# Kernel optimization log

Hardware: AMD Instinct MI355X
Metric: run time of the kernel (lower is better)

Reference implementation:

```python
import jax, jax.numpy as jnp
import numpy as np

D_MODEL = 1024
N_HEAD = 16
HEAD_D = D_MODEL // N_HEAD
D_FF = 4096
LN_EPS = 1e-5
ATTN_EPS = 1e-6


def _layer_norm(x, g, b, eps=LN_EPS):
    mu = jnp.mean(x, axis=-1, keepdims=True)
    var = jnp.var(x, axis=-1, keepdims=True)
    return (x - mu) * jax.lax.rsqrt(var + eps) * g + b


def setup_inputs() -> dict:
    key = jax.random.key(0)
    ks = jax.random.split(key, 16)
    s = 0.02
    return {
        "src": jax.random.normal(ks[0], (4, 4096, D_MODEL), dtype=jnp.float32),
        "qkv_w": jax.random.normal(ks[1], (D_MODEL, 3 * D_MODEL), dtype=jnp.float32) * s,
        "qkv_b": jax.random.normal(ks[2], (3 * D_MODEL,), dtype=jnp.float32) * s,
        "out_w": jax.random.normal(ks[3], (D_MODEL, D_MODEL), dtype=jnp.float32) * s,
        "out_b": jax.random.normal(ks[4], (D_MODEL,), dtype=jnp.float32) * s,
        "w1": jax.random.normal(ks[5], (D_MODEL, D_FF), dtype=jnp.float32) * s,
        "b1": jax.random.normal(ks[6], (D_FF,), dtype=jnp.float32) * s,
        "w2": jax.random.normal(ks[7], (D_FF, D_MODEL), dtype=jnp.float32) * s,
        "b2": jax.random.normal(ks[8], (D_MODEL,), dtype=jnp.float32) * s,
        "g1": jnp.ones((D_MODEL,), dtype=jnp.float32),
        "be1": jnp.zeros((D_MODEL,), dtype=jnp.float32),
        "g2": jnp.ones((D_MODEL,), dtype=jnp.float32),
        "be2": jnp.zeros((D_MODEL,), dtype=jnp.float32),
    }


def _linear_attention(x, qkv_w, qkv_b, out_w, out_b):
    B, N, C = x.shape
    qkv = (x @ qkv_w + qkv_b).reshape(B, N, 3, N_HEAD, HEAD_D)
    qkv = jnp.transpose(qkv, (2, 0, 3, 1, 4))  # [3,B,H,N,D]
    q, k, v = qkv[0], qkv[1], qkv[2]
    # phi = elu(x) + 1 (positive feature map)
    qf = jax.nn.elu(q) + 1.0
    kf = jax.nn.elu(k) + 1.0
    # kv aggregation: [B,H,D,D]
    kv = jnp.einsum('bhnd,bhne->bhde', kf.astype(jnp.float32), v.astype(jnp.float32)).astype(v.dtype)
    y_num = jnp.einsum('bhnd,bhde->bhne', qf, kv)  # [B,H,N,D]
    z = jnp.sum(kf.astype(jnp.float32), axis=2)  # [B,H,D]
    y_den = jnp.einsum('bhnd,bhd->bhn', qf, z.astype(qf.dtype))
    y_den = jnp.maximum(y_den, ATTN_EPS)[..., None]
    y = (y_num / y_den).transpose(0, 2, 1, 3).reshape(B, N, C)
    return y @ out_w + out_b


def reference(src, qkv_w, qkv_b, out_w, out_b, w1, b1, w2, b2, g1, be1, g2, be2):
    # pre-norm (norm_first=True), dropout disabled (eval)
    attn_out = _linear_attention(_layer_norm(src, g1, be1), qkv_w, qkv_b, out_w, out_b)
    x = src + attn_out
    h = jax.nn.gelu(_layer_norm(x, g2, be2) @ w1 + b1, approximate=False)
    return x + h @ w2 + b2
```

## Files before the change

kernel.cpp:

```cpp
#include <hip/hip_runtime.h>
#include <hip/hip_bf16.h>
#include <math.h>

typedef __attribute__((ext_vector_type(8))) short short8;
typedef __attribute__((ext_vector_type(4))) float floatx4;

__device__ __forceinline__ float bf2f(unsigned int u) {
    union { unsigned int i; float f; } c; c.i = u << 16; return c.f;
}
__device__ __forceinline__ unsigned short f2bf(float f) {
    unsigned int x = __builtin_bit_cast(unsigned int, f);
    unsigned int r = (x + 0x7fffu + ((x >> 16) & 1u)) >> 16;
    return (unsigned short)r;
}
__device__ __forceinline__ float elu1(float x) { return x > 0.f ? x + 1.f : __expf(x); }
__device__ __forceinline__ float gelu_fast(float x) {
    float u = x * (1.f + 0.044715f * x * x);
    return x / (1.f + __expf(-1.5957691216f * u));
}

__device__ __forceinline__ void async_cp16(const void* g, void* l) {
    __builtin_amdgcn_global_load_lds(
        (const __attribute__((address_space(1))) unsigned int*)g,
        (__attribute__((address_space(3))) unsigned int*)l, 16, 0, 0);
}

__global__ void prep_kernel(const float* __restrict__ qkv_w, const float* __restrict__ out_w,
                            const float* __restrict__ w1, const float* __restrict__ w2,
                            unsigned short* __restrict__ qkvwT, unsigned short* __restrict__ outwT,
                            unsigned short* __restrict__ w1T, unsigned short* __restrict__ w2T,
                            float* __restrict__ kvz,
                            const float* __restrict__ src, const float* __restrict__ g1,
                            const float* __restrict__ be1, unsigned short* __restrict__ ln1out) {
    const int bid = blockIdx.x;
    const int tx = threadIdx.x, ty = threadIdx.y;
    const int lid = ty * 32 + tx;
    if (bid >= 12548) {
        const int row = bid - 12548;
        const int t = lid;
        const float4 v = *(const float4*)(src + (size_t)row * 1024 + t * 4);
        float s = v.x + v.y + v.z + v.w;
        float s2 = v.x * v.x + v.y * v.y + v.z * v.z + v.w * v.w;
#pragma unroll
        for (int off = 32; off > 0; off >>= 1) {
            s += __shfl_down(s, off);
            s2 += __shfl_down(s2, off);
        }
        __shared__ float red[8];
        __shared__ float stat[2];
        const int w = t >> 6, l = t & 63;
        if (l == 0) { red[w] = s; red[4 + w] = s2; }
        __syncthreads();
        if (t == 0) {
            float S = red[0] + red[1] + red[2] + red[3];
            float S2 = red[4] + red[5] + red[6] + red[7];
            float mu = S * (1.f / 1024.f);
            float var = S2 * (1.f / 1024.f) - mu * mu;
            stat[0] = mu;
            stat[1] = rsqrtf(var + 1e-5f);
        }
        __syncthreads();
        const float mu = stat[0], rs = stat[1];
        const float4 gv = *(const float4*)(g1 + t * 4);
        const float4 bv = *(const float4*)(be1 + t * 4);
        uint2 pk;
        pk.x = (unsigned int)f2bf((v.x - mu) * rs * gv.x + bv.x) |
               ((unsigned int)f2bf((v.y - mu) * rs * gv.y + bv.y) << 16);
        pk.y = (unsigned int)f2bf((v.z - mu) * rs * gv.z + bv.z) |
               ((unsigned int)f2bf((v.w - mu) * rs * gv.w + bv.w) << 16);
        *(uint2*)(ln1out + (size_t)row * 1024 + t * 4) = pk;
        return;
    }
    if (bid >= 12288) {
        const int i = (bid - 12288) * 1024 + lid * 4;
        *(float4*)(kvz + i) = make_float4(0.f, 0.f, 0.f, 0.f);
        return;
    }
    const float* in;
    unsigned short* op;
    int K, N, tb;
    if (bid < 3072)      { in = qkv_w; op = qkvwT; K = 1024; N = 3072; tb = bid; }
    else if (bid < 4096) { in = out_w; op = outwT; K = 1024; N = 1024; tb = bid - 3072; }
    else if (bid < 8192) { in = w1;    op = w1T;   K = 1024; N = 4096; tb = bid - 4096; }
    else                 { in = w2;    op = w2T;   K = 4096; N = 1024; tb = bid - 8192; }
    const int nx = N >> 5;
    const int n0 = (tb % nx) * 32, k0 = (tb / nx) * 32;
    __shared__ float tile[32][33];
#pragma unroll
    for (int i = 0; i < 4; i++)
        tile[ty + 8 * i][tx] = in[(size_t)(k0 + ty + 8 * i) * N + n0 + tx];
    __syncthreads();
#pragma unroll
    for (int i = 0; i < 4; i++)
        op[(size_t)(n0 + ty + 8 * i) * K + k0 + tx] = f2bf(tile[tx][ty + 8 * i]);
}

__global__ __launch_bounds__(256)
void ln_kernel(const unsigned short* __restrict__ x, const float* __restrict__ g,
               const float* __restrict__ be, unsigned short* __restrict__ out) {
    const int row = blockIdx.x;
    const int t = threadIdx.x;
    float4 v;
    {
        uint2 r = *(const uint2*)(x + (size_t)row * 1024 + t * 4);
        v.x = bf2f(r.x & 0xffff); v.y = bf2f(r.x >> 16);
        v.z = bf2f(r.y & 0xffff); v.w = bf2f(r.y >> 16);
    }
    float s = v.x + v.y + v.z + v.w;
    float s2 = v.x * v.x + v.y * v.y + v.z * v.z + v.w * v.w;
#pragma unroll
    for (int off = 32; off > 0; off >>= 1) {
        s += __shfl_down(s, off);
        s2 += __shfl_down(s2, off);
    }
    __shared__ float red[8];
    __shared__ float stat[2];
    const int w = t >> 6, l = t & 63;
    if (l == 0) { red[w] = s; red[4 + w] = s2; }
    __syncthreads();
    if (t == 0) {
        float S = red[0] + red[1] + red[2] + red[3];
        float S2 = red[4] + red[5] + red[6] + red[7];
        float mu = S * (1.f / 1024.f);
        float var = S2 * (1.f / 1024.f) - mu * mu;
        stat[0] = mu;
        stat[1] = rsqrtf(var + 1e-5f);
    }
    __syncthreads();
    const float mu = stat[0], rs = stat[1];
    const float4 gv = *(const float4*)(g + t * 4);
    const float4 bv = *(const float4*)(be + t * 4);
    uint2 pk;
    pk.x = (unsigned int)f2bf((v.x - mu) * rs * gv.x + bv.x) |
           ((unsigned int)f2bf((v.y - mu) * rs * gv.y + bv.y) << 16);
    pk.y = (unsigned int)f2bf((v.z - mu) * rs * gv.z + bv.z) |
           ((unsigned int)f2bf((v.w - mu) * rs * gv.w + bv.w) << 16);
    *(uint2*)(out + (size_t)row * 1024 + t * 4) = pk;
}

template <int EPI>
__global__ __launch_bounds__(256, 4)
void gemm_bt(const unsigned short* __restrict__ A, const unsigned short* __restrict__ B,
             const float* __restrict__ bias, const float* __restrict__ resid,
             const unsigned short* __restrict__ residb,
             unsigned short* __restrict__ Cbf, float* __restrict__ Cf32,
             int N, int K) {
    __shared__ __align__(16) unsigned char smem[33792];
    unsigned short* At = (unsigned short*)smem;
    unsigned short* Bt = (unsigned short*)(smem + 16384);
    const int t = threadIdx.x;
    const int l = t & 63;
    const int w = t >> 6;

    const int f = blockIdx.y * gridDim.x + blockIdx.x;
    int bx = blockIdx.x, by = blockIdx.y;
    if (gridDim.y == 128 && (gridDim.x & 3) == 0) {
        const int xcd = f & 7;
        const int g = f >> 3;
        const int nin = g & 3;
        const int r = (g >> 2) & 15;
        const int nchunk = g >> 6;
        bx = nchunk * 4 + nin;
        by = xcd * 16 + r;
    }
    const int m0 = by * 128;
    const int n0 = bx * 128;
    const int wm = (w >> 1) * 64;
    const int wn = (w & 1) * 64;

    floatx4 acc[4][4];
    const floatx4 zz = {0.f, 0.f, 0.f, 0.f};
#pragma unroll
    for (int i = 0; i < 4; i++)
#pragma unroll
        for (int j = 0; j < 4; j++) acc[i][j] = zz;

    const int sr = t >> 3;
    const int sg = ((t & 7) ^ ((t >> 3) & 7));
    const unsigned short* ag = A + (size_t)(m0 + sr) * K + sg * 8;
    const unsigned short* bg = B + (size_t)(n0 + sr) * K + sg * 8;
    unsigned short* la = At + t * 8;
    unsigned short* lb = Bt + t * 8;

    const int fr = l & 15;
    const int fx = fr & 7;
    const int g0 = (l >> 4);

    for (int k0 = 0; k0 < K; k0 += 64) {
#pragma unroll
        for (int c = 0; c < 4; c++) {
            async_cp16(ag + k0 + (size_t)(c * 32) * K, la + c * 2048);
            async_cp16(bg + k0 + (size_t)(c * 32) * K, lb + c * 2048);
        }
        __syncthreads();
#pragma unroll
        for (int sub = 0; sub < 2; sub++) {
            const int fo = ((sub * 4 + g0) ^ fx) << 3;
            short8 af[4], bf[4];
#pragma unroll
            for (int i = 0; i < 4; i++)
                af[i] = *(const short8*)(At + (wm + i * 16 + fr) * 64 + fo);
#pragma unroll
            for (int i = 0; i < 4; i++)
                bf[i] = *(const short8*)(Bt + (wn + i * 16 + fr) * 64 + fo);
#pragma unroll
            for (int i = 0; i < 4; i++)
#pragma unroll
                for (int j = 0; j < 4; j++)
                    acc[i][j] = __builtin_amdgcn_mfma_f32_16x16x32_bf16(af[i], bf[j], acc[i][j], 0, 0, 0);
        }
        __syncthreads();
    }

    const int er = (l >> 4) << 2;
    const int ec = l & 15;

    if (EPI != 4) {
        unsigned short* Ct = (unsigned short*)smem;
#pragma unroll
        for (int j = 0; j < 4; j++) {
            const int lcol = wn + j * 16 + ec;
            const float bb = bias[n0 + lcol];
#pragma unroll
            for (int i = 0; i < 4; i++) {
                const int lrowb = wm + i * 16 + er;
#pragma unroll
                for (int r = 0; r < 4; r++) {
                    float v = acc[i][j][r] + bb;
                    if (EPI == 0) { if (n0 + lcol < 2048) v = elu1(v); }
                    if (EPI == 2) v = gelu_fast(v);
                    Ct[(lrowb + r) * 132 + lcol] = f2bf(v);
                }
            }
        }
        __syncthreads();
        const int srow = t >> 4;
        const int scol = (t & 15) * 8;
#pragma unroll
        for (int it = 0; it < 8; it++) {
            const int lrow = it * 16 + srow;
            uint4 d = *(const uint4*)(Ct + lrow * 132 + scol);
            if (EPI == 3) {
                const float* rp = resid + (size_t)(m0 + lrow) * N + n0 + scol;
                float4 r0 = *(const float4*)rp;
                float4 r1 = *(const float4*)(rp + 4);
                uint4 o;
                o.x = (unsigned int)f2bf(bf2f(d.x & 0xffff) + r0.x) |
                      ((unsigned int)f2bf(bf2f(d.x >> 16) + r0.y) << 16);
                o.y = (unsigned int)f2bf(bf2f(d.y & 0xffff) + r0.z) |
                      ((unsigned int)f2bf(bf2f(d.y >> 16) + r0.w) << 16);
                o.z = (unsigned int)f2bf(bf2f(d.z & 0xffff) + r1.x) |
                      ((unsigned int)f2bf(bf2f(d.z >> 16) + r1.y) << 16);
                o.w = (unsigned int)f2bf(bf2f(d.w & 0xffff) + r1.z) |
                      ((unsigned int)f2bf(bf2f(d.w >> 16) + r1.w) << 16);
                d = o;
            }
            *(uint4*)(Cbf + (size_t)(m0 + lrow) * N + n0 + scol) = d;
        }
    } else {
        float* Cf = (float*)smem;
#pragma unroll
        for (int half = 0; half < 2; half++) {
            if ((w >> 1) == half) {
#pragma unroll
                for (int j = 0; j < 4; j++) {
                    const int lcol = wn + j * 16 + ec;
                    const float bb = bias[n0 + lcol];
#pragma unroll
                    for (int i = 0; i < 4; i++) {
                        const int lrow = i * 16 + er;
#pragma unroll
                        for (int r = 0; r < 4; r++)
                            Cf[(lrow + r) * 132 + lcol] = acc[i][j][r] + bb;
                    }
                }
            }
            __syncthreads();
            const int srow = t >> 5;
            const int scol = (t & 31) * 4;
#pragma unroll
            for (int it = 0; it < 8; it++) {
                const int lrow = it * 8 + srow;
                const int grow = m0 + half * 64 + lrow;
                float4 v4 = *(const float4*)(Cf + lrow * 132 + scol);
                uint2 rb = *(const uint2*)(residb + (size_t)grow * N + n0 + scol);
                v4.x += bf2f(rb.x & 0xffff);
                v4.y += bf2f(rb.x >> 16);
                v4.z += bf2f(rb.y & 0xffff);
                v4.w += bf2f(rb.y >> 16);
                *(float4*)(Cf32 + (size_t)grow * N + n0 + scol) = v4;
            }
            __syncthreads();
        }
    }
}

__global__ __launch_bounds__(256)
void kv_kernel(const unsigned short* __restrict__ qkv, float* __restrict__ kvz) {
    const int bh = blockIdx.x;
    const int chunk = blockIdx.y;
    const int b = bh >> 4, h = bh & 15;
    const int t = threadIdx.x;
    __shared__ float kf[64][68];
    __shared__ float vv[64][68];
    const int te = t >> 4, td = t & 15;
    float acc[4][4];
#pragma unroll
    for (int i = 0; i < 4; i++)
#pragma unroll
        for (int j = 0; j < 4; j++) acc[i][j] = 0.f;
    float zacc = 0.f;
    const size_t base = (size_t)b * 4096 * 3072 + (size_t)chunk * 512 * 3072;
    const int koff = 1024 + h * 64;
    const int voff = 2048 + h * 64;
    const int rl = t >> 3, seg = t & 7;

    for (int s = 0; s < 8; s++) {
#pragma unroll
        for (int p = 0; p < 2; p++) {
            const int nl = p * 32 + rl;
            const unsigned short* rp = qkv + base + (size_t)(s * 64 + nl) * 3072;
            const uint4 kd = *(const uint4*)(rp + koff + seg * 8);
            const uint4 vd = *(const uint4*)(rp + voff + seg * 8);
            float* kdst = &kf[nl][seg * 8];
            float* vdst = &vv[nl][seg * 8];
            kdst[0] = bf2f(kd.x & 0xffff); kdst[1] = bf2f(kd.x >> 16);
            kdst[2] = bf2f(kd.y & 0xffff); kdst[3] = bf2f(kd.y >> 16);
            kdst[4] = bf2f(kd.z & 0xffff); kdst[5] = bf2f(kd.z >> 16);
            kdst[6] = bf2f(kd.w & 0xffff); kdst[7] = bf2f(kd.w >> 16);
            vdst[0] = bf2f(vd.x & 0xffff); vdst[1] = bf2f(vd.x >> 16);
            vdst[2] = bf2f(vd.y & 0xffff); vdst[3] = bf2f(vd.y >> 16);
            vdst[4] = bf2f(vd.z & 0xffff); vdst[5] = bf2f(vd.z >> 16);
            vdst[6] = bf2f(vd.w & 0xffff); vdst[7] = bf2f(vd.w >> 16);
        }
        __syncthreads();
        for (int n = 0; n < 64; n++) {
            const float4 kk = *(const float4*)&kf[n][te * 4];
            const float4 vn = *(const float4*)&vv[n][td * 4];
            const float ka[4] = {kk.x, kk.y, kk.z, kk.w};
            const float va[4] = {vn.x, vn.y, vn.z, vn.w};
#pragma unroll
            for (int i = 0; i < 4; i++)
#pragma unroll
                for (int j = 0; j < 4; j++) acc[i][j] = fmaf(ka[i], va[j], acc[i][j]);
        }
        if (t < 64) {
            for (int n = 0; n < 64; n++) zacc += kf[n][t];
        }
        __syncthreads();
    }
    float* kvp = kvz + bh * 4160;
#pragma unroll
    for (int i = 0; i < 4; i++)
#pragma unroll
        for (int j = 0; j < 4; j++)
            atomicAdd(&kvp[(te * 4 + i) * 64 + td * 4 + j], acc[i][j]);
    if (t < 64) atomicAdd(&kvp[4096 + t], zacc);
}

__global__ __launch_bounds__(256)
void y_kernel(const unsigned short* __restrict__ qkv, const float* __restrict__ kvz,
              unsigned short* __restrict__ y) {
    const int bh = blockIdx.x, chunk = blockIdx.y;
    const int b = bh >> 4, h = bh & 15;
    const int t = threadIdx.x;
    __shared__ float kv[64][68];
    __shared__ float zs[64];
    __shared__ float qf[16][68];
    const float* kvp = kvz + bh * 4160;
#pragma unroll
    for (int p = 0; p < 4; p++) {
        const int f = (t + p * 256) * 4;
        const float4 v4 = *(const float4*)(kvp + f);
        *(float4*)&kv[f >> 6][f & 63] = v4;
    }
    if (t < 16) *(float4*)&zs[t * 4] = *(const float4*)(kvp + 4096 + t * 4);
    __syncthreads();
    const int nl = t >> 4, td = t & 15;
    const size_t base = (size_t)b * 4096 * 3072 + (size_t)chunk * 128 * 3072;
    const int qoff = h * 64;
    for (int s = 0; s < 8; s++) {
        if (t < 128) {
            const int r = t >> 3, seg = t & 7;
            const uint4 qd = *(const uint4*)(qkv + base + (size_t)(s * 16 + r) * 3072 + qoff + seg * 8);
            float* qdst = &qf[r][seg * 8];
            qdst[0] = bf2f(qd.x & 0xffff); qdst[1] = bf2f(qd.x >> 16);
            qdst[2] = bf2f(qd.y & 0xffff); qdst[3] = bf2f(qd.y >> 16);
            qdst[4] = bf2f(qd.z & 0xffff); qdst[5] = bf2f(qd.z >> 16);
            qdst[6] = bf2f(qd.w & 0xffff); qdst[7] = bf2f(qd.w >> 16);
        }
        __syncthreads();
        float a0 = 0.f, a1 = 0.f, a2 = 0.f, a3 = 0.f, den = 0.f;
        for (int e = 0; e < 64; e++) {
            const float q = qf[nl][e];
            const float4 kvv = *(const float4*)&kv[e][td * 4];
            a0 = fmaf(q, kvv.x, a0);
            a1 = fmaf(q, kvv.y, a1);
            a2 = fmaf(q, kvv.z, a2);
            a3 = fmaf(q, kvv.w, a3);
            den = fmaf(q, zs[e], den);
        }
        const float inv = 1.f / fmaxf(den, 1e-6f);
        const int tok = b * 4096 + chunk * 128 + s * 16 + nl;
        uint2 pk;
        pk.x = (unsigned int)f2bf(a0 * inv) | ((unsigned int)f2bf(a1 * inv) << 16);
        pk.y = (unsigned int)f2bf(a2 * inv) | ((unsigned int)f2bf(a3 * inv) << 16);
        *(uint2*)(y + (size_t)tok * 1024 + h * 64 + td * 4) = pk;
        __syncthreads();
    }
}

extern "C" void kernel_launch(void* const* d_in, const int* in_sizes, int n_in,
                              void* d_out, int out_size, void* d_ws, size_t ws_size,
                              hipStream_t stream) {
    const float* src   = (const float*)d_in[0];
    const float* qkv_w = (const float*)d_in[1];
    const float* qkv_b = (const float*)d_in[2];
    const float* out_w = (const float*)d_in[3];
    const float* out_b = (const float*)d_in[4];
    const float* w1    = (const float*)d_in[5];
    const float* b1    = (const float*)d_in[6];
    const float* w2    = (const float*)d_in[7];
    const float* b2    = (const float*)d_in[8];
    const float* g1    = (const float*)d_in[9];
    const float* be1   = (const float*)d_in[10];
    const float* g2    = (const float*)d_in[11];
    const float* be2   = (const float*)d_in[12];
    float* outp = (float*)d_out;

    char* ws = (char*)d_ws;
    unsigned short* qkvwT = (unsigned short*)(ws + 0);
    unsigned short* outwT = (unsigned short*)(ws + 6291456);
    unsigned short* w1T   = (unsigned short*)(ws + 8388608);
    unsigned short* w2T   = (unsigned short*)(ws + 16777216);
    unsigned short* bufA  = (unsigned short*)(ws + 25165824);
    unsigned short* bufB  = (unsigned short*)(ws + 159383552);
    unsigned short* xbuf  = (unsigned short*)(ws + 192937984);
    float*          kvz   = (float*)(ws + 260046848);

    prep_kernel<<<28932, dim3(32, 8), 0, stream>>>(qkv_w, out_w, w1, w2,
                                                   qkvwT, outwT, w1T, w2T, kvz,
                                                   src, g1, be1, bufB);

    gemm_bt<0><<<dim3(24, 128), 256, 0, stream>>>(bufB, qkvwT, qkv_b, nullptr, nullptr, bufA, nullptr, 3072, 1024);
    kv_kernel<<<dim3(64, 8), 256, 0, stream>>>(bufA, kvz);
    y_kernel<<<dim3(64, 32), 256, 0, stream>>>(bufA, kvz, bufB);
    gemm_bt<3><<<dim3(8, 128), 256, 0, stream>>>(bufB, outwT, out_b, src, nullptr, xbuf, nullptr, 1024, 1024);
    ln_kernel<<<16384, 256, 0, stream>>>(xbuf, g2, be2, bufB);
    gemm_bt<2><<<dim3(32, 128), 256, 0, stream>>>(bufB, w1T, b1, nullptr, nullptr, bufA, nullptr, 4096, 1024);
    gemm_bt<4><<<dim3(8, 128), 256, 0, stream>>>(bufA, w2T, b2, nullptr, xbuf, nullptr, outp, 1024, 4096);
}
```

Before: 789.4 us.

## Replace direct-to-LDS loads with register-staged double-buffered GEMM pipeline

The GEMM main loop drops the global_load_lds async copies with a single LDS buffer and two barriers per K step. It now prefetches BK=32 tiles into registers, writes them into one of two LDS buffers while the other is consumed by MFMA, and uses one lgkmcnt wait plus barrier per step. The swizzle changes to suit 32-element rows, and launch bounds drop to 3 waves per SIMD to make room for the extra staging registers. The aim is to overlap global loads with compute and halve barrier count, at the cost of register pressure, lower occupancy and more LDS store instructions.

```diff
diff --git a/kernel.cpp b/kernel.cpp
--- a/kernel.cpp
+++ b/kernel.cpp
@@ -19,10 +19,8 @@
     return x / (1.f + __expf(-1.5957691216f * u));
 }
 
-__device__ __forceinline__ void async_cp16(const void* g, void* l) {
-    __builtin_amdgcn_global_load_lds(
-        (const __attribute__((address_space(1))) unsigned int*)g,
-        (__attribute__((address_space(3))) unsigned int*)l, 16, 0, 0);
+__device__ __forceinline__ void lgkm_barrier() {
+    asm volatile("s_waitcnt lgkmcnt(0)\n\ts_barrier" ::: "memory");
 }
 
 __global__ void prep_kernel(const float* __restrict__ qkv_w, const float* __restrict__ out_w,
@@ -139,15 +137,15 @@
 }
 
 template <int EPI>
-__global__ __launch_bounds__(256, 4)
+__global__ __launch_bounds__(256, 3)
 void gemm_bt(const unsigned short* __restrict__ A, const unsigned short* __restrict__ B,
              const float* __restrict__ bias, const float* __restrict__ resid,
              const unsigned short* __restrict__ residb,
              unsigned short* __restrict__ Cbf, float* __restrict__ Cf32,
              int N, int K) {
     __shared__ __align__(16) unsigned char smem[33792];
-    unsigned short* At = (unsigned short*)smem;
-    unsigned short* Bt = (unsigned short*)(smem + 16384);
+    unsigned short* smu = (unsigned short*)smem;
+    const unsigned short* sm = smu;
     const int t = threadIdx.x;
     const int l = t & 63;
     const int w = t >> 6;
@@ -175,48 +173,87 @@
 #pragma unroll
         for (int j = 0; j < 4; j++) acc[i][j] = zz;
 
-    const int sr = t >> 3;
-    const int sg = ((t & 7) ^ ((t >> 3) & 7));
-    const unsigned short* ag = A + (size_t)(m0 + sr) * K + sg * 8;
-    const unsigned short* bg = B + (size_t)(n0 + sr) * K + sg * 8;
-    unsigned short* la = At + t * 8;
-    unsigned short* lb = Bt + t * 8;
+    const int sr = t >> 2;
+    const int sg = t & 3;
+    const int sp = sg ^ (sr & 3);
+    const int lwa = sr * 32 + sp * 8;
+    const unsigned short* agl = A + (size_t)(m0 + sr) * K + sg * 8;
+    const unsigned short* bgl = B + (size_t)(n0 + sr) * K + sg * 8;
+    const size_t rowK64 = (size_t)64 * K;
 
     const int fr = l & 15;
-    const int fx = fr & 7;
-    const int g0 = (l >> 4);
-
-    for (int k0 = 0; k0 < K; k0 += 64) {
-#pragma unroll
-        for (int c = 0; c < 4; c++) {
-            async_cp16(ag + k0 + (size_t)(c * 32) * K, la + c * 2048);
-            async_cp16(bg + k0 + (size_t)(c * 32) * K, lb + c * 2048);
-        }
-        __syncthreads();
-#pragma unroll
-        for (int sub = 0; sub < 2; sub++) {
-            const int fo = ((sub * 4 + g0) ^ fx) << 3;
-            short8 af[4], bf[4];
-#pragma unroll
-            for (int i = 0; i < 4; i++)
-                af[i] = *(const short8*)(At + (wm + i * 16 + fr) * 64 + fo);
-#pragma unroll
-            for (int i = 0; i < 4; i++)
-                bf[i] = *(const short8*)(Bt + (wn + i * 16 + fr) * 64 + fo);
-#pragma unroll
-            for (int i = 0; i < 4; i++)
-#pragma unroll
-                for (int j = 0; j < 4; j++)
-                    acc[i][j] = __builtin_amdgcn_mfma_f32_16x16x32_bf16(af[i], bf[j], acc[i][j], 0, 0, 0);
-        }
-        __syncthreads();
-    }
+    const int foE = (((l >> 4) ^ (l & 3)) << 3);
+
+#define COMPUTE(BUF) do { \
+    const unsigned short* base_ = sm + (BUF) * 8192; \
+    short8 af[4], bfr[4]; \
+    _Pragma("unroll") for (int i_ = 0; i_ < 4; i_++) \
+        af[i_] = *(const short8*)(base_ + (wm + i_ * 16 + fr) * 32 + foE); \
+    _Pragma("unroll") for (int i_ = 0; i_ < 4; i_++) \
+        bfr[i_] = *(const short8*)(base_ + 4096 + (wn + i_ * 16 + fr) * 32 + foE); \
+    _Pragma("unroll") for (int i_ = 0; i_ < 4; i_++) \
+    _Pragma("unroll") for (int j_ = 0; j_ < 4; j_++) \
+        acc[i_][j_] = __builtin_amdgcn_mfma_f32_16x16x32_bf16(af[i_], bfr[j_], acc[i_][j_], 0, 0, 0); \
+} while (0)
+
+#define COMMIT(BUF, A0, A1, B0, B1) do { \
+    unsigned short* d_ = smu + (BUF) * 8192; \
+    *(uint4*)(d_ + lwa) = (A0); \
+    *(uint4*)(d_ + lwa + 2048) = (A1); \
+    *(uint4*)(d_ + 4096 + lwa) = (B0); \
+    *(uint4*)(d_ + 4096 + lwa + 2048) = (B1); \
+} while (0)
+
+    const int T = K >> 5;
+    uint4 ra0, ra1, rb0, rb1, sa0, sa1, sb0, sb1;
+
+    ra0 = *(const uint4*)(agl);
+    ra1 = *(const uint4*)(agl + rowK64);
+    rb0 = *(const uint4*)(bgl);
+    rb1 = *(const uint4*)(bgl + rowK64);
+    COMMIT(0, ra0, ra1, rb0, rb1);
+    sa0 = *(const uint4*)(agl + 32);
+    sa1 = *(const uint4*)(agl + rowK64 + 32);
+    sb0 = *(const uint4*)(bgl + 32);
+    sb1 = *(const uint4*)(bgl + rowK64 + 32);
+    lgkm_barrier();
+
+    for (int tk = 0; tk < T - 2; tk += 2) {
+        {
+            const int ko = (tk + 2) * 32;
+            ra0 = *(const uint4*)(agl + ko);
+            ra1 = *(const uint4*)(agl + rowK64 + ko);
+            rb0 = *(const uint4*)(bgl + ko);
+            rb1 = *(const uint4*)(bgl + rowK64 + ko);
+        }
+        COMPUTE(0);
+        COMMIT(1, sa0, sa1, sb0, sb1);
+        lgkm_barrier();
+        {
+            const int ko = (tk + 3) * 32;
+            sa0 = *(const uint4*)(agl + ko);
+            sa1 = *(const uint4*)(agl + rowK64 + ko);
+            sb0 = *(const uint4*)(bgl + ko);
+            sb1 = *(const uint4*)(bgl + rowK64 + ko);
+        }
+        COMPUTE(1);
+        COMMIT(0, ra0, ra1, rb0, rb1);
+        lgkm_barrier();
+    }
+    COMPUTE(0);
+    COMMIT(1, sa0, sa1, sb0, sb1);
+    lgkm_barrier();
+    COMPUTE(1);
+    lgkm_barrier();
+
+#undef COMPUTE
+#undef COMMIT
 
     const int er = (l >> 4) << 2;
     const int ec = l & 15;
 
     if (EPI != 4) {
-        unsigned short* Ct = (unsigned short*)smem;
+        unsigned short* Ct = smu;
 #pragma unroll
         for (int j = 0; j < 4; j++) {
             const int lcol = wn + j * 16 + ec;
```

Measured after the change: 840.7 us. +6.5%, slower.
